# Performance work log

Measured on AMD Instinct MI355X. Metric: run time of the kernel, lower is better.

## Reference

```python
import jax, jax.numpy as jnp
import numpy as np

EPS = 1e-5  # torch BatchNorm1d default eps


def _bn(x, axes):
    # BatchNorm in training mode with gamma=1, beta=0 (torch init values):
    # normalize with biased batch statistics over the given axes.
    m = x.mean(axes, keepdims=True)
    v = x.var(axes, keepdims=True)
    return (x - m) * jax.lax.rsqrt(v + EPS)


def setup_inputs() -> dict:
    key = jax.random.key(0)
    ks = jax.random.split(key, 12)
    N, M = 50000, 12
    OF, F, E, H = 92, 64, 41, 128
    Z = 2 * F + E  # 169 = concat(node, nbr_node, edge)

    def w(k, shape, fan):
        return jax.random.normal(k, shape, jnp.float32) * np.float32(1.0 / np.sqrt(fan))

    return {
        "node_fea": jax.random.normal(ks[0], (N, OF), jnp.float32),
        "edge_fea": jax.random.uniform(ks[1], (N, M, E), dtype=jnp.float32),
        "nbr_offset": jax.random.randint(ks[2], (N, M, 3), -1, 2).astype(jnp.float32),
        "atom_pos": jax.random.uniform(ks[3], (N, 3), dtype=jnp.float32) * 10.0,
        "cells": jnp.broadcast_to(jnp.eye(3, dtype=jnp.float32) * 10.0, (N, 3, 3))
                 + jax.random.normal(ks[4], (N, 3, 3), jnp.float32) * 0.1,
        "edge_idx": jax.random.randint(ks[5], (N, M), 0, N),
        "W_emb": w(ks[6], (OF, F), OF), "b_emb": jnp.zeros((F,), jnp.float32),
        "W_pre_node": w(ks[7], (3, Z, 2 * F), Z), "b_pre_node": jnp.zeros((3, 2 * F), jnp.float32),
        "W_pre_edge": w(ks[8], (3, Z, 2 * E), Z), "b_pre_edge": jnp.zeros((3, 2 * E), jnp.float32),
        "W_dist": w(ks[9], (Z, H), Z), "b_dist": jnp.zeros((H,), jnp.float32),
        "W_const": w(ks[10], (Z, H), Z), "b_const": jnp.zeros((H,), jnp.float32),
    }


def reference(node_fea, edge_fea, nbr_offset, atom_pos, cells, edge_idx,
              W_emb, b_emb, W_pre_node, b_pre_node, W_pre_edge, b_pre_edge,
              W_dist, b_dist, W_const, b_const):
    N, M = edge_idx.shape
    lrelu = jax.nn.leaky_relu  # torch LeakyReLU default slope 0.01
    sig = jax.nn.sigmoid
    sp = jax.nn.softplus

    # get_distance: neighbor Cartesian positions via unit-cell offsets
    off_cart = jnp.einsum('nmi,nij->nmj', nbr_offset, cells)         # (N,M,3)
    diff = atom_pos[edge_idx] + off_cart - atom_pos[:, None, :]       # (N,M,3)
    distance = jnp.sqrt(jnp.sum(diff * diff, -1, keepdims=True) + 1e-12)  # (N,M,1)

    node = node_fea @ W_emb + b_emb  # embedding -> (N,64)

    for l in range(W_pre_node.shape[0]):  # n_conv = 3 ConvLayers
        nbr = node[edge_idx]  # gather (N,M,F)
        z = jnp.concatenate(
            [jnp.broadcast_to(node[:, None, :], (N, M, node.shape[-1])), nbr, edge_fea],
            axis=2)  # (N,M,169)
        # node branch: linear -> BN -> sigmoid*leakyrelu gate -> sum over M -> BN -> residual
        zn = _bn(z @ W_pre_node[l] + b_pre_node[l], (0, 1))  # (N,M,128)
        nf, nc = jnp.split(zn, 2, axis=2)
        aggr = jnp.sum(sig(nf) * lrelu(nc), axis=1)           # (N,64)
        node = lrelu(node + _bn(aggr, (0,)))
        # edge branch: linear -> BN -> gate -> BN -> residual
        ze = _bn(z @ W_pre_edge[l] + b_pre_edge[l], (0, 1))   # (N,M,82)
        ef, ec = jnp.split(ze, 2, axis=2)
        edge_fea = lrelu(edge_fea + _bn(sig(ef) * lrelu(ec), (0, 1)))

    nbr = node[edge_idx]
    bond_fea = jnp.concatenate(
        [jnp.broadcast_to(node[:, None, :], (N, M, node.shape[-1])), nbr, edge_fea],
        axis=2)  # (N,M,169)

    # n_h_dist == 1 branch: softplus(BN(linear) + distance), mean over channels
    bd = sp(_bn(bond_fea @ W_dist + b_dist, (0, 1)) + distance)
    bd = jnp.mean(bd, axis=2, keepdims=True)                  # (N,M,1)
    # n_h_const == 1 branch: softplus(BN(linear)), mean over channels, / N
    bc = sp(_bn(bond_fea @ W_const + b_const, (0, 1)))
    bc = jnp.mean(bc, axis=2, keepdims=True) / N              # (N,M,1)

    return jnp.concatenate([bd, bc], axis=2)                  # (N,M,2)
```

## Files before the change

### kernel.cpp

```cpp
#include <hip/hip_runtime.h>
#include <math.h>

#define NN 50000
#define MM 12
#define NM 600000
#define OF 92
#define FF 64
#define EE 41
#define ES 48
#define ZZ 169
#define RPB 96
#define NPB 8
#define NBLK 6250
#define KP 200
#define KSTEPS 6
#define MT 6
#define NSLICE 64
#define PSTRIDE 1024
#define TPB 512

typedef __bf16 bf16x8 __attribute__((ext_vector_type(8)));
typedef float  f32x4  __attribute__((ext_vector_type(4)));

__device__ __forceinline__ float lrelu(float x){ return fmaxf(x, 0.01f*x); }
__device__ __forceinline__ float sigm(float x){ return __builtin_amdgcn_rcpf(1.f+__expf(-x)); }
__device__ __forceinline__ float softpl(float x){ return fmaxf(x,0.f) + __logf(1.f+__expf(-fabsf(x))); }
__device__ __forceinline__ unsigned short f2bf(float f){
    __bf16 h = (__bf16)f;
    return __builtin_bit_cast(unsigned short, h);
}
__device__ __forceinline__ float b2f(unsigned short u){
    unsigned int b = ((unsigned int)u) << 16;
    return __builtin_bit_cast(float, b);
}

__global__ __launch_bounds__(256) void pack_w(const float* __restrict__ Wn,
    const float* __restrict__ We, const float* __restrict__ Wd,
    const float* __restrict__ Wc, unsigned short* __restrict__ dst)
{
    int idx = blockIdx.x*256 + threadIdx.x;
    if (idx >= 4*49152) return;
    int j    = idx & 7;
    int lane = (idx >> 3) & 63;
    int ntks = (idx >> 9) % 96;
    int L    = idx / 49152;
    int nt = ntks & 15, ks = ntks >> 4;
    int k   = ks*32 + (lane>>4)*8 + j;
    int col = nt*16 + (lane&15);
    float v = 0.f;
    if (k < ZZ) {
        if (L < 3) {
            if (col < 128)                       v = Wn[((size_t)L*ZZ + k)*128 + col];
            else if (col >= 128 && col < 128+EE) v = We[((size_t)L*ZZ + k)*82 + (col-128)];
            else if (col >= 192 && col < 192+EE) v = We[((size_t)L*ZZ + k)*82 + 41 + (col-192)];
        } else {
            if (col < 128) v = Wd[(size_t)k*128 + col];
            else           v = Wc[(size_t)k*128 + (col-128)];
        }
    }
    dst[idx] = f2bf(v);
}

__global__ __launch_bounds__(256) void k_dist(const float* __restrict__ off,
    const float* __restrict__ apos, const float* __restrict__ cells,
    const int* __restrict__ eidx, float* __restrict__ distb)
{
    int idx = blockIdx.x*256 + threadIdx.x;
    if (idx >= NM) return;
    int n = idx / MM;
    const float* o  = off + (size_t)idx*3;
    const float* cl = cells + (size_t)n*9;
    int n2 = eidx[idx];
    float o0=o[0], o1=o[1], o2=o[2];
    float dd = 1e-12f;
    #pragma unroll
    for (int j=0;j<3;j++){
        float oc = o0*cl[0*3+j] + o1*cl[1*3+j] + o2*cl[2*3+j];
        float d = apos[(size_t)n2*3+j] + oc - apos[(size_t)n*3+j];
        dd += d*d;
    }
    distb[idx] = sqrtf(dd);
}

__global__ __launch_bounds__(256) void k_cvt(const float* __restrict__ src,
    unsigned short* __restrict__ e)
{
    int idx = blockIdx.x*256 + threadIdx.x;
    if (idx >= NM*ES) return;
    int gr = idx / ES;
    int c  = idx - gr*ES;
    e[idx] = (c < EE) ? f2bf(src[(size_t)gr*EE + c]) : (unsigned short)0;
}

__global__ __launch_bounds__(256) void k_emb(const float* __restrict__ nf,
    const float* __restrict__ W, const float* __restrict__ b,
    unsigned short* __restrict__ node0)
{
    int idx = blockIdx.x*256 + threadIdx.x;
    if (idx >= NN*FF) return;
    int n = idx >> 6, c = idx & 63;
    float s = b[c];
    for (int k=0;k<OF;k++) s = fmaf(nf[(size_t)n*OF+k], W[k*FF+c], s);
    node0[idx] = f2bf(s);
}

__global__ __launch_bounds__(256) void k_red(float* __restrict__ P,
    float* __restrict__ dst, int lo, int hi)
{
    for (int c = lo + threadIdx.x; c < hi; c += 256) {
        float s = 0.f;
        #pragma unroll 8
        for (int sl = 0; sl < NSLICE; ++sl) s += P[sl*PSTRIDE + c];
        dst[c] = s;
        #pragma unroll 8
        for (int sl = 0; sl < NSLICE; ++sl) P[sl*PSTRIDE + c] = 0.f;
    }
}

__device__ __forceinline__ void stage_z(unsigned short* __restrict__ Zl,
    const unsigned short* __restrict__ node_src, const unsigned short* __restrict__ edge_src,
    const int* __restrict__ eidx, int n0, int tid)
{
    const int gr0 = n0 * MM;
    const int r0 = tid >> 3, ch = tid & 7;
    const bool two = tid < 256;
    const int r1 = r0 + 64;
    const int e0 = eidx[gr0 + r0];
    const int e1 = two ? eidx[gr0 + r1] : 0;
    const int na0 = n0 + r0 / MM;
    const int na1 = n0 + r1 / MM;
    const uint4 z4 = make_uint4(0u,0u,0u,0u);
    uint4 s0  = *(const uint4*)(node_src + (size_t)na0*FF + ch*8);
    uint4 nb0 = *(const uint4*)(node_src + (size_t)e0*FF + ch*8);
    uint4 d0 = z4, s1 = z4, nb1 = z4, d1 = z4;
    if (ch < 6) d0 = *(const uint4*)(edge_src + (size_t)(gr0+r0)*ES + ch*8);
    if (two) {
        s1  = *(const uint4*)(node_src + (size_t)na1*FF + ch*8);
        nb1 = *(const uint4*)(node_src + (size_t)e1*FF + ch*8);
        if (ch < 6) d1 = *(const uint4*)(edge_src + (size_t)(gr0+r1)*ES + ch*8);
    }
    *(uint4*)(Zl + r0*KP + ch*8)        = s0;
    *(uint4*)(Zl + r0*KP + 64 + ch*8)   = nb0;
    *(uint4*)(Zl + r0*KP + 128 + ch*8)  = d0;
    if (two) {
        *(uint4*)(Zl + r1*KP + ch*8)       = s1;
        *(uint4*)(Zl + r1*KP + 64 + ch*8)  = nb1;
        *(uint4*)(Zl + r1*KP + 128 + ch*8) = d1;
    }
}

__device__ __forceinline__ void mfma_core(const unsigned short* __restrict__ Zl,
    const unsigned short* __restrict__ Wpk, int h, int sw, int lane, f32x4 (&acc)[MT][2])
{
    const int quad = lane >> 4, li = lane & 15;
    #pragma unroll
    for (int mt=0;mt<MT;mt++){
        acc[mt][0] = (f32x4){0.f,0.f,0.f,0.f};
        acc[mt][1] = (f32x4){0.f,0.f,0.f,0.f};
    }
    const int nt0 = h*8 + sw;
    #pragma unroll 2
    for (int ks=0; ks<KSTEPS; ++ks) {
        bf16x8 bfr0 = *(const bf16x8*)(Wpk + (((ks*16 + nt0    )*64 + lane) << 3));
        bf16x8 bfr1 = *(const bf16x8*)(Wpk + (((ks*16 + nt0 + 4)*64 + lane) << 3));
        bf16x8 afr[MT];
        #pragma unroll
        for (int mt=0;mt<MT;mt++)
            afr[mt] = *(const bf16x8*)(Zl + (mt*16+li)*KP + ks*32 + quad*8);
        #pragma unroll
        for (int mt=0;mt<MT;mt++){
            acc[mt][0] = __builtin_amdgcn_mfma_f32_16x16x32_bf16(afr[mt], bfr0, acc[mt][0], 0, 0, 0);
            acc[mt][1] = __builtin_amdgcn_mfma_f32_16x16x32_bf16(afr[mt], bfr1, acc[mt][1], 0, 0, 0);
        }
    }
}

__device__ __forceinline__ void stats_epi(const f32x4 (&acc)[MT][2], int h, int sw, int lane,
    float* __restrict__ Ps)
{
    const int quad = lane>>4, li = lane&15;
    #pragma unroll
    for (int t=0;t<2;t++){
        float s=0.f, q=0.f;
        #pragma unroll
        for (int mt=0;mt<MT;mt++)
            #pragma unroll
            for (int r=0;r<4;r++){ float v = acc[mt][t][r]; s+=v; q = fmaf(v,v,q); }
        s += __shfl_xor(s,16); s += __shfl_xor(s,32);
        q += __shfl_xor(q,16); q += __shfl_xor(q,32);
        if (quad == 0) {
            int col = h*128 + t*64 + sw*16 + li;
            atomicAdd(&Ps[col], s);
            atomicAdd(&Ps[256+col], q);
        }
    }
}

__global__ __launch_bounds__(TPB,3) void k_stats(
    const unsigned short* __restrict__ node_src, const unsigned short* __restrict__ edge_src,
    const int* __restrict__ eidx, const unsigned short* __restrict__ Wpk,
    float* __restrict__ Pst)
{
    __shared__ unsigned short Zl[RPB*KP];
    const int tid = threadIdx.x, w = tid>>6, lane = tid&63;
    const int h = w>>2, sw = w&3;
    const int n0 = blockIdx.x * NPB;
    stage_z(Zl, node_src, edge_src, eidx, n0, tid);
    __syncthreads();
    f32x4 acc[MT][2];
    mfma_core(Zl, Wpk, h, sw, lane, acc);
    float* Ps = Pst + (size_t)(blockIdx.x & (NSLICE-1))*PSTRIDE;
    stats_epi(acc, h, sw, lane, Ps);
}

__global__ __launch_bounds__(TPB,3) void k_apply_re(
    const unsigned short* __restrict__ node_src, const unsigned short* __restrict__ edge_src,
    const int* __restrict__ eidx, const unsigned short* __restrict__ Wpk,
    const float* __restrict__ preS, const float* __restrict__ preQ,
    float* __restrict__ aggr, unsigned short* __restrict__ gbuf,
    float* __restrict__ Pst)
{
    __shared__ __align__(16) char smem[RPB*KP*2];
    unsigned short* Zl = (unsigned short*)smem;
    float* gL = (float*)smem;
    const int tid = threadIdx.x, w = tid>>6, lane = tid&63;
    const int quad = lane>>4, li = lane&15;
    const int h = w>>2, sw = w&3;
    const int n0 = blockIdx.x * NPB;
    const int gr0 = n0 * MM;
    stage_z(Zl, node_src, edge_src, eidx, n0, tid);
    __syncthreads();
    f32x4 acc[MT][2];
    mfma_core(Zl, Wpk, h, sw, lane, acc);
    __syncthreads();

    const int cg0 = sw*16 + li;
    float sc[2], bi[2];
    #pragma unroll
    for (int t=0;t<2;t++){
        int col = h*128 + t*64 + cg0;
        float mm = preS[col]*(1.f/(float)NM);
        float vv = preQ[col]*(1.f/(float)NM) - mm*mm;
        float is = rsqrtf(vv + 1e-5f);
        sc[t] = is; bi[t] = -mm*is;
    }
    float* Ps = Pst + (size_t)(blockIdx.x & (NSLICE-1))*PSTRIDE;

    if (h == 0) {
        #pragma unroll
        for (int mt=0;mt<MT;mt++)
            #pragma unroll
            for (int r=0;r<4;r++){
                int row = mt*16 + quad*4 + r;
                float nf = fmaf(acc[mt][0][r], sc[0], bi[0]);
                float nc = fmaf(acc[mt][1][r], sc[1], bi[1]);
                gL[row*68 + cg0] = sigm(nf) * lrelu(nc);
            }
    } else {
        const bool ce_ok = cg0 < EE;
        float pg = 0.f, pq = 0.f;
        #pragma unroll
        for (int mt=0;mt<MT;mt++)
            #pragma unroll
            for (int r=0;r<4;r++){
                int row = mt*16 + quad*4 + r;
                float ef = fmaf(acc[mt][0][r], sc[0], bi[0]);
                float ec = fmaf(acc[mt][1][r], sc[1], bi[1]);
                float gv = sigm(ef)*lrelu(ec);
                if (ce_ok) {
                    gbuf[(size_t)(gr0+row)*ES + cg0] = f2bf(gv);
                    pg += gv; pq = fmaf(gv,gv,pq);
                }
            }
        pg += __shfl_xor(pg,16); pg += __shfl_xor(pg,32);
        pq += __shfl_xor(pq,16); pq += __shfl_xor(pq,32);
        if (quad==0 && ce_ok){ atomicAdd(&Ps[640+cg0], pg); atomicAdd(&Ps[704+cg0], pq); }
    }
    __syncthreads();
    {
        float vsum = 0.f;
        #pragma unroll
        for (int jj=0;jj<MM;jj++) vsum += gL[(w*MM+jj)*68 + lane];
        aggr[(size_t)(n0+w)*64 + lane] = vsum;
        atomicAdd(&Ps[512+lane], vsum);
        atomicAdd(&Ps[576+lane], vsum*vsum);
    }
}

__global__ __launch_bounds__(256) void k_upd_node(const unsigned short* __restrict__ cur,
    const float* __restrict__ aggr, const float* __restrict__ aS,
    const float* __restrict__ aQ, unsigned short* __restrict__ nxt)
{
    int idx = blockIdx.x*256 + threadIdx.x;
    if (idx >= NN*8) return;
    int n = idx >> 3, ch = idx & 7;
    int base = n*64 + ch*8;
    float4 a0 = *(const float4*)(aggr + base);
    float4 a1 = *(const float4*)(aggr + base + 4);
    uint4 cu = *(const uint4*)(cur + base);
    unsigned short cs[8]; *(uint4*)cs = cu;
    float av[8] = {a0.x,a0.y,a0.z,a0.w,a1.x,a1.y,a1.z,a1.w};
    unsigned short os[8];
    #pragma unroll
    for (int j=0;j<8;j++){
        int c = ch*8+j;
        float mm = aS[c]*(1.f/(float)NN);
        float vv = aQ[c]*(1.f/(float)NN) - mm*mm;
        float is = rsqrtf(vv + 1e-5f);
        float v = (av[j] - mm) * is;
        os[j] = f2bf(lrelu(b2f(cs[j]) + v));
    }
    *(uint4*)(nxt + base) = *(uint4*)os;
}

__global__ __launch_bounds__(256) void k_upd_edge(unsigned short* __restrict__ e,
    const unsigned short* __restrict__ g, const float* __restrict__ gS,
    const float* __restrict__ gQ)
{
    int idx = blockIdx.x*256 + threadIdx.x;
    if (idx >= NM*6) return;
    int gr = idx / 6, ch = idx - gr*6;
    size_t base = (size_t)gr*ES + ch*8;
    uint4 eu = *(const uint4*)(e + base);
    uint4 gu = *(const uint4*)(g + base);
    unsigned short es8[8], gs8[8], os[8];
    *(uint4*)es8 = eu; *(uint4*)gs8 = gu;
    #pragma unroll
    for (int j=0;j<8;j++){
        int c = ch*8+j;
        if (c < EE) {
            float mm = gS[c]*(1.f/(float)NM);
            float vv = gQ[c]*(1.f/(float)NM) - mm*mm;
            float is = rsqrtf(vv + 1e-5f);
            float v = (b2f(gs8[j]) - mm) * is;
            os[j] = f2bf(lrelu(b2f(es8[j]) + v));
        } else {
            os[j] = es8[j];
        }
    }
    *(uint4*)(e + base) = *(uint4*)os;
}

__global__ __launch_bounds__(TPB,3) void k_final_re(
    const unsigned short* __restrict__ node_src, const unsigned short* __restrict__ edge_src,
    const int* __restrict__ eidx, const unsigned short* __restrict__ Wpk,
    const float* __restrict__ fS, const float* __restrict__ fQ,
    const float* __restrict__ distb, float* __restrict__ out)
{
    __shared__ __align__(16) char smem[RPB*KP*2];
    unsigned short* Zl = (unsigned short*)smem;
    float* bufD = (float*)smem;
    float* bufC = (float*)(smem + 8192);
    const int tid = threadIdx.x, w = tid>>6, lane = tid&63;
    const int quad = lane>>4, li = lane&15;
    const int h = w>>2, sw = w&3;
    const int n0 = blockIdx.x * NPB;
    const int gr0 = n0 * MM;
    stage_z(Zl, node_src, edge_src, eidx, n0, tid);
    __syncthreads();
    f32x4 acc[MT][2];
    mfma_core(Zl, Wpk, h, sw, lane, acc);
    __syncthreads();

    const int cg0 = sw*16 + li;
    float sc[2], bi[2];
    #pragma unroll
    for (int t=0;t<2;t++){
        int col = h*128 + t*64 + cg0;
        float mm = fS[col]*(1.f/(float)NM);
        float vv = fQ[col]*(1.f/(float)NM) - mm*mm;
        float is = rsqrtf(vv + 1e-5f);
        sc[t] = is; bi[t] = -mm*is;
    }
    const int liq = li >> 2;
    const bool wr = (li & 3) == 0;
    float* buf = (h == 0) ? bufD : bufC;
    #pragma unroll
    for (int mt=0;mt<MT;mt++)
        #pragma unroll
        for (int r=0;r<4;r++){
            int row = mt*16 + quad*4 + r;
            float v0 = fmaf(acc[mt][0][r], sc[0], bi[0]);
            float v1 = fmaf(acc[mt][1][r], sc[1], bi[1]);
            float p;
            if (h == 0) {
                float dv = distb[gr0 + row];
                p = softpl(v0 + dv) + softpl(v1 + dv);
            } else {
                p = softpl(v0) + softpl(v1);
            }
            p += __shfl_xor(p,1); p += __shfl_xor(p,2);
            if (wr) buf[row*17 + sw*4 + liq] = p;
        }
    __syncthreads();
    if (tid < 2*RPB) {
        int hh = tid >= RPB;
        int row = tid - (hh ? RPB : 0);
        const float* bsrc = hh ? bufC : bufD;
        float s = 0.f;
        #pragma unroll
        for (int t=0;t<16;t++) s += bsrc[row*17+t];
        size_t gr = gr0 + row;
        out[gr*2 + hh] = hh ? s * (1.f/128.f) * (1.f/(float)NN) : s * (1.f/128.f);
    }
}

extern "C" void kernel_launch(void* const* d_in, const int* in_sizes, int n_in,
                              void* d_out, int out_size, void* d_ws, size_t ws_size,
                              hipStream_t stream)
{
    const float* node_fea = (const float*)d_in[0];
    const float* edge_in  = (const float*)d_in[1];
    const float* nbr_off  = (const float*)d_in[2];
    const float* apos     = (const float*)d_in[3];
    const float* cells    = (const float*)d_in[4];
    const int*   eidx     = (const int*)  d_in[5];
    const float* W_emb    = (const float*)d_in[6];
    const float* b_emb    = (const float*)d_in[7];
    const float* W_pn     = (const float*)d_in[8];
    const float* W_pe     = (const float*)d_in[10];
    const float* W_dist   = (const float*)d_in[12];
    const float* W_cst    = (const float*)d_in[14];
    float* out = (float*)d_out;
    char* ws = (char*)d_ws;

    size_t o = 0;
    auto alloc = [&](size_t bytes) { char* p = ws + o; o += (bytes + 255) & ~(size_t)255; return p; };
    unsigned short* node0 = (unsigned short*)alloc((size_t)NN*FF*2);
    unsigned short* node1 = (unsigned short*)alloc((size_t)NN*FF*2);
    unsigned short* ebuf  = (unsigned short*)alloc((size_t)NM*ES*2);
    unsigned short* gbuf  = (unsigned short*)alloc((size_t)NM*ES*2);
    float* aggr  = (float*)alloc((size_t)NN*FF*4);
    float* distb = (float*)alloc((size_t)NM*4);
    unsigned short* Wpk = (unsigned short*)alloc((size_t)4*49152*2);
    float* stats = (float*)alloc(4096*4);
    float* Pst   = (float*)alloc((size_t)NSLICE*PSTRIDE*4);

    hipMemsetAsync(stats, 0, 4096*sizeof(float), stream);
    hipMemsetAsync(Pst, 0, (size_t)NSLICE*PSTRIDE*sizeof(float), stream);
    pack_w<<<(4*49152+255)/256, 256, 0, stream>>>(W_pn, W_pe, W_dist, W_cst, Wpk);
    k_dist <<<(NM+255)/256,     256, 0, stream>>>(nbr_off, apos, cells, eidx, distb);
    k_cvt  <<<(NM*ES+255)/256,  256, 0, stream>>>(edge_in, ebuf);
    k_emb  <<<(NN*FF+255)/256,  256, 0, stream>>>(node_fea, W_emb, b_emb, node0);

    const unsigned short* ncur = node0;

    for (int l=0;l<3;l++){
        float* st = stats + l*768;
        float* preS = st;       float* preQ = st+256;
        float* aSs  = st+512;   float* aQq  = st+576;
        float* gSs  = st+640;   float* gQq  = st+704;
        const unsigned short* Wl = Wpk + (size_t)l*49152;
        unsigned short* ndst = (l & 1) ? node0 : node1;

        k_stats  <<<NBLK,TPB,0,stream>>>(ncur, ebuf, eidx, Wl, Pst);
        k_red    <<<1,256,0,stream>>>(Pst, st, 0, 512);
        k_apply_re<<<NBLK,TPB,0,stream>>>(ncur, ebuf, eidx, Wl, preS, preQ,
                                          aggr, gbuf, Pst);
        k_red    <<<1,256,0,stream>>>(Pst, st, 512, 768);
        k_upd_node<<<(NN*8+255)/256,256,0,stream>>>(ncur, aggr, aSs, aQq, ndst);
        k_upd_edge<<<(NM*6+255)/256,256,0,stream>>>(ebuf, gbuf, gSs, gQq);
        ncur = ndst;
    }

    float* fSt = stats + 3*768;
    float* fS = fSt; float* fQ = fSt + 256;
    const unsigned short* Wf = Wpk + (size_t)3*49152;
    k_stats  <<<NBLK,TPB,0,stream>>>(ncur, ebuf, eidx, Wf, Pst);
    k_red    <<<1,256,0,stream>>>(Pst, fSt, 0, 512);
    k_final_re<<<NBLK,TPB,0,stream>>>(ncur, ebuf, eidx, Wf, fS, fQ, distb, out);
}
```

Baseline: 1.239 ms.

## Fuse edge BN update into stats staging and process two tiles per block

The separate edge-update kernel is removed. The edge residual BN update now runs inside the next layer's stats kernel while it stages the Z tile, and the updated edge features are written back to the edge buffer there. Each block now handles two 96-row tiles, prefetching the second tile's global loads into registers while the MFMAs for the first run, and atomics are accumulated across both tiles before being issued. This saves a full pass over the edge buffer and halves the block count. In exchange it raises register pressure from the eight uint4 prefetch registers and adds extra barriers.

```diff
diff --git a/kernel.cpp b/kernel.cpp
--- a/kernel.cpp
+++ b/kernel.cpp
@@ -11,7 +11,8 @@
 #define ZZ 169
 #define RPB 96
 #define NPB 8
-#define NBLK 6250
+#define NTILE 6250
+#define NBLK2 3125
 #define KP 200
 #define KSTEPS 6
 #define MT 6
@@ -117,46 +118,91 @@
     }
 }
 
-__device__ __forceinline__ void stage_z(unsigned short* __restrict__ Zl,
-    const unsigned short* __restrict__ node_src, const unsigned short* __restrict__ edge_src,
-    const int* __restrict__ eidx, int n0, int tid)
+__device__ __forceinline__ void stage_load(uint4* __restrict__ R,
+    const unsigned short* __restrict__ node_src, const unsigned short* __restrict__ ebuf,
+    const unsigned short* __restrict__ gbuf, const int* __restrict__ eidx,
+    int n0, int tid, bool upd)
 {
     const int gr0 = n0 * MM;
     const int r0 = tid >> 3, ch = tid & 7;
     const bool two = tid < 256;
-    const int r1 = r0 + 64;
-    const int e0 = eidx[gr0 + r0];
-    const int e1 = two ? eidx[gr0 + r1] : 0;
-    const int na0 = n0 + r0 / MM;
-    const int na1 = n0 + r1 / MM;
     const uint4 z4 = make_uint4(0u,0u,0u,0u);
-    uint4 s0  = *(const uint4*)(node_src + (size_t)na0*FF + ch*8);
-    uint4 nb0 = *(const uint4*)(node_src + (size_t)e0*FF + ch*8);
-    uint4 d0 = z4, s1 = z4, nb1 = z4, d1 = z4;
-    if (ch < 6) d0 = *(const uint4*)(edge_src + (size_t)(gr0+r0)*ES + ch*8);
+    int e0 = eidx[gr0 + r0];
+    R[0] = *(const uint4*)(node_src + (size_t)(n0 + r0/MM)*FF + ch*8);
+    R[1] = *(const uint4*)(node_src + (size_t)e0*FF + ch*8);
+    R[2] = z4; R[3] = z4; R[4] = z4; R[5] = z4; R[6] = z4; R[7] = z4;
+    if (ch < 6) {
+        R[2] = *(const uint4*)(ebuf + (size_t)(gr0+r0)*ES + ch*8);
+        if (upd) R[3] = *(const uint4*)(gbuf + (size_t)(gr0+r0)*ES + ch*8);
+    }
     if (two) {
-        s1  = *(const uint4*)(node_src + (size_t)na1*FF + ch*8);
-        nb1 = *(const uint4*)(node_src + (size_t)e1*FF + ch*8);
-        if (ch < 6) d1 = *(const uint4*)(edge_src + (size_t)(gr0+r1)*ES + ch*8);
-    }
-    *(uint4*)(Zl + r0*KP + ch*8)        = s0;
-    *(uint4*)(Zl + r0*KP + 64 + ch*8)   = nb0;
-    *(uint4*)(Zl + r0*KP + 128 + ch*8)  = d0;
+        int r1 = r0 + 64;
+        int e1 = eidx[gr0 + r1];
+        R[4] = *(const uint4*)(node_src + (size_t)(n0 + r1/MM)*FF + ch*8);
+        R[5] = *(const uint4*)(node_src + (size_t)e1*FF + ch*8);
+        if (ch < 6) {
+            R[6] = *(const uint4*)(ebuf + (size_t)(gr0+r1)*ES + ch*8);
+            if (upd) R[7] = *(const uint4*)(gbuf + (size_t)(gr0+r1)*ES + ch*8);
+        }
+    }
+}
+
+__device__ __forceinline__ uint4 upd_edge8(uint4 e, uint4 g,
+    const float* __restrict__ mmv, const float* __restrict__ isv, int ch)
+{
+    unsigned short es[8], gs[8], os[8];
+    *(uint4*)es = e; *(uint4*)gs = g;
+    #pragma unroll
+    for (int j=0;j<8;j++){
+        int c = ch*8+j;
+        if (c < EE){
+            float v = (b2f(gs[j]) - mmv[j]) * isv[j];
+            os[j] = f2bf(lrelu(b2f(es[j]) + v));
+        } else os[j] = es[j];
+    }
+    return *(uint4*)os;
+}
+
+__device__ __forceinline__ void stage_write(uint4* __restrict__ R,
+    unsigned short* __restrict__ Zl, unsigned short* __restrict__ ebuf_wb,
+    int n0, int tid, bool upd,
+    const float* __restrict__ mmv, const float* __restrict__ isv)
+{
+    const int gr0 = n0 * MM;
+    const int r0 = tid >> 3, ch = tid & 7;
+    const bool two = tid < 256;
+    uint4 d0 = R[2];
+    if (upd && ch < 6) {
+        d0 = upd_edge8(R[2], R[3], mmv, isv, ch);
+        *(uint4*)(ebuf_wb + (size_t)(gr0+r0)*ES + ch*8) = d0;
+    }
+    *(uint4*)(Zl + r0*KP + ch*8)       = R[0];
+    *(uint4*)(Zl + r0*KP + 64 + ch*8)  = R[1];
+    *(uint4*)(Zl + r0*KP + 128 + ch*8) = d0;
     if (two) {
-        *(uint4*)(Zl + r1*KP + ch*8)       = s1;
-        *(uint4*)(Zl + r1*KP + 64 + ch*8)  = nb1;
+        int r1 = r0 + 64;
+        uint4 d1 = R[6];
+        if (upd && ch < 6) {
+            d1 = upd_edge8(R[6], R[7], mmv, isv, ch);
+            *(uint4*)(ebuf_wb + (size_t)(gr0+r1)*ES + ch*8) = d1;
+        }
+        *(uint4*)(Zl + r1*KP + ch*8)       = R[4];
+        *(uint4*)(Zl + r1*KP + 64 + ch*8)  = R[5];
         *(uint4*)(Zl + r1*KP + 128 + ch*8) = d1;
     }
 }
 
+template<bool ZERO>
 __device__ __forceinline__ void mfma_core(const unsigned short* __restrict__ Zl,
     const unsigned short* __restrict__ Wpk, int h, int sw, int lane, f32x4 (&acc)[MT][2])
 {
     const int quad = lane >> 4, li = lane & 15;
-    #pragma unroll
-    for (int mt=0;mt<MT;mt++){
-        acc[mt][0] = (f32x4){0.f,0.f,0.f,0.f};
-        acc[mt][1] = (f32x4){0.f,0.f,0.f,0.f};
+    if (ZERO) {
+        #pragma unroll
+        for (int mt=0;mt<MT;mt++){
+            acc[mt][0] = (f32x4){0.f,0.f,0.f,0.f};
+            acc[mt][1] = (f32x4){0.f,0.f,0.f,0.f};
+        }
     }
     const int nt0 = h*8 + sw;
     #pragma unroll 2
@@ -197,24 +243,49 @@
 }
 
 __global__ __launch_bounds__(TPB,3) void k_stats(
-    const unsigned short* __restrict__ node_src, const unsigned short* __restrict__ edge_src,
-    const int* __restrict__ eidx, const unsigned short* __restrict__ Wpk,
+    const unsigned short* __restrict__ node_src, unsigned short* __restrict__ ebuf,
+    const unsigned short* __restrict__ gbuf, const int* __restrict__ eidx,
+    const unsigned short* __restrict__ Wpk,
+    const float* __restrict__ gS, const float* __restrict__ gQ,
     float* __restrict__ Pst)
 {
     __shared__ unsigned short Zl[RPB*KP];
     const int tid = threadIdx.x, w = tid>>6, lane = tid&63;
     const int h = w>>2, sw = w&3;
-    const int n0 = blockIdx.x * NPB;
-    stage_z(Zl, node_src, edge_src, eidx, n0, tid);
+    const bool upd = (gS != nullptr);
+    const int ch = tid & 7;
+    float mmv[8], isv[8];
+    if (upd) {
+        #pragma unroll
+        for (int j=0;j<8;j++){
+            int c = ch*8+j;
+            float mm = 0.f, is = 0.f;
+            if (c < EE) {
+                mm = gS[c]*(1.f/(float)NM);
+                float vv = gQ[c]*(1.f/(float)NM) - mm*mm;
+                is = rsqrtf(vv + 1e-5f);
+            }
+            mmv[j] = mm; isv[j] = is;
+        }
+    }
+    const int t0 = blockIdx.x * 2;
+    uint4 R[8];
+    stage_load(R, node_src, ebuf, gbuf, eidx, t0*NPB, tid, upd);
+    stage_write(R, Zl, ebuf, t0*NPB, tid, upd, mmv, isv);
     __syncthreads();
+    stage_load(R, node_src, ebuf, gbuf, eidx, (t0+1)*NPB, tid, upd);
     f32x4 acc[MT][2];
-    mfma_core(Zl, Wpk, h, sw, lane, acc);
+    mfma_core<true>(Zl, Wpk, h, sw, lane, acc);
+    __syncthreads();
+    stage_write(R, Zl, ebuf, (t0+1)*NPB, tid, upd, mmv, isv);
+    __syncthreads();
+    mfma_core<false>(Zl, Wpk, h, sw, lane, acc);
     float* Ps = Pst + (size_t)(blockIdx.x & (NSLICE-1))*PSTRIDE;
     stats_epi(acc, h, sw, lane, Ps);
 }
 
 __global__ __launch_bounds__(TPB,3) void k_apply_re(
-    const unsigned short* __restrict__ node_src, const unsigned short* __restrict__ edge_src,
+    const unsigned short* __restrict__ node_src, const unsigned short* __restrict__ ebuf,
     const int* __restrict__ eidx, const unsigned short* __restrict__ Wpk,
     const float* __restrict__ preS, const float* __restrict__ preQ,
     float* __restrict__ aggr, unsigned short* __restrict__ gbuf,
@@ -226,13 +297,13 @@
     const int tid = threadIdx.x, w = tid>>6, lane = tid&63;
     const int quad = lane>>4, li = lane&15;
     const int h = w>>2, sw = w&3;
-    const int n0 = blockIdx.x * NPB;
-    const int gr0 = n0 * MM;
-    stage_z(Zl, node_src, edge_src, eidx, n0, tid);
+    const int t0 = blockIdx.x * 2;
+
+    uint4 R[8];
+    stage_load(R, node_src, ebuf, nullptr, eidx, t0*NPB, tid, false);
+    stage_write(R, Zl, nullptr, t0*NPB, tid, false, nullptr, nullptr);
     __syncthreads();
-    f32x4 acc[MT][2];
-    mfma_core(Zl, Wpk, h, sw, lane, acc);
-    __syncthreads();
+    stage_load(R, node_src, ebuf, nullptr, eidx, (t0+1)*NPB, tid, false);
 
     const int cg0 = sw*16 + li;
     float sc[2], bi[2];
@@ -244,47 +315,62 @@
         float is = rsqrtf(vv + 1e-5f);
         sc[t] = is; bi[t] = -mm*is;
     }
+    const bool ce_ok = cg0 < EE;
     float* Ps = Pst + (size_t)(blockIdx.x & (NSLICE-1))*PSTRIDE;
-
-    if (h == 0) {
-        #pragma unroll
-        for (int mt=0;mt<MT;mt++)
+    float pg = 0.f, pq = 0.f;
+    float sAcc = 0.f, sQq = 0.f;
+
+    f32x4 acc[MT][2];
+    #pragma unroll
+    for (int tile=0; tile<2; ++tile){
+        const int n0 = (t0+tile)*NPB;
+        const int gr0 = n0 * MM;
+        mfma_core<true>(Zl, Wpk, h, sw, lane, acc);
+        __syncthreads();
+        if (h == 0) {
             #pragma unroll
-            for (int r=0;r<4;r++){
-                int row = mt*16 + quad*4 + r;
-                float nf = fmaf(acc[mt][0][r], sc[0], bi[0]);
-                float nc = fmaf(acc[mt][1][r], sc[1], bi[1]);
-                gL[row*68 + cg0] = sigm(nf) * lrelu(nc);
-            }
-    } else {
-        const bool ce_ok = cg0 < EE;
-        float pg = 0.f, pq = 0.f;
-        #pragma unroll
-        for (int mt=0;mt<MT;mt++)
+            for (int mt=0;mt<MT;mt++)
+                #pragma unroll
+                for (int r=0;r<4;r++){
+                    int row = mt*16 + quad*4 + r;
+                    float nf = fmaf(acc[mt][0][r], sc[0], bi[0]);
+                    float nc = fmaf(acc[mt][1][r], sc[1], bi[1]);
+                    gL[row*68 + cg0] = sigm(nf) * lrelu(nc);
+                }
+        } else {
             #pragma unroll
-            for (int r=0;r<4;r++){
-                int row = mt*16 + quad*4 + r;
-                float ef = fmaf(acc[mt][0][r], sc[0], bi[0]);
-                float ec = fmaf(acc[mt][1][r], sc[1], bi[1]);
-                float gv = sigm(ef)*lrelu(ec);
-                if (ce_ok) {
-                    gbuf[(size_t)(gr0+row)*ES + cg0] = f2bf(gv);
-                    pg += gv; pq = fmaf(gv,gv,pq);
+            for (int mt=0;mt<MT;mt++)
+                #pragma unroll
+                for (int r=0;r<4;r++){
+                    int row = mt*16 + quad*4 + r;
+                    float ef = fmaf(acc[mt][0][r], sc[0], bi[0]);
+                    float ec = fmaf(acc[mt][1][r], sc[1], bi[1]);
+                    float gv = sigm(ef)*lrelu(ec);
+                    if (ce_ok) {
+                        gbuf[(size_t)(gr0+row)*ES + cg0] = f2bf(gv);
+                        pg += gv; pq = fmaf(gv,gv,pq);
+                    }
                 }
-            }
-        pg += __shfl_xor(pg,16); pg += __shfl_xor(pg,32);
-        pq += __shfl_xor(pq,16); pq += __shfl_xor(pq,32);
-        if (quad==0 && ce_ok){ atomicAdd(&Ps[640+cg0], pg); atomicAdd(&Ps[704+cg0], pq); }
-    }
-    __syncthreads();
-    {
-        float vsum = 0.f;
-        #pragma unroll
-        for (int jj=0;jj<MM;jj++) vsum += gL[(w*MM+jj)*68 + lane];
-        aggr[(size_t)(n0+w)*64 + lane] = vsum;
-        atomicAdd(&Ps[512+lane], vsum);
-        atomicAdd(&Ps[576+lane], vsum*vsum);
-    }
+        }
+        __syncthreads();
+        {
+            float vsum = 0.f;
+            #pragma unroll
+            for (int jj=0;jj<MM;jj++) vsum += gL[(w*MM+jj)*68 + lane];
+            aggr[(size_t)(n0+w)*64 + lane] = vsum;
+            sAcc += vsum; sQq = fmaf(vsum,vsum,sQq);
+        }
+        if (tile == 0) {
+            __syncthreads();
+            stage_write(R, Zl, nullptr, (t0+1)*NPB, tid, false, nullptr, nullptr);
+            __syncthreads();
+        }
+    }
+    pg += __shfl_xor(pg,16); pg += __shfl_xor(pg,32);
+    pq += __shfl_xor(pq,16); pq += __shfl_xor(pq,32);
+    if (h==1 && quad==0 && ce_ok){ atomicAdd(&Ps[640+cg0], pg); atomicAdd(&Ps[704+cg0], pq); }
+    atomicAdd(&Ps[512+lane], sAcc);
+    atomicAdd(&Ps[576+lane], sQq);
 }
 
 __global__ __launch_bounds__(256) void k_upd_node(const unsigned short* __restrict__ cur,
@@ -313,36 +399,8 @@
     *(uint4*)(nxt + base) = *(uint4*)os;
 }
 
-__global__ __launch_bounds__(256) void k_upd_edge(unsigned short* __restrict__ e,
-    const unsigned short* __restrict__ g, const float* __restrict__ gS,
-    const float* __restrict__ gQ)
-{
-    int idx = blockIdx.x*256 + threadIdx.x;
-    if (idx >= NM*6) return;
-    int gr = idx / 6, ch = idx - gr*6;
-    size_t base = (size_t)gr*ES + ch*8;
-    uint4 eu = *(const uint4*)(e + base);
-    uint4 gu = *(const uint4*)(g + base);
-    unsigned short es8[8], gs8[8], os[8];
-    *(uint4*)es8 = eu; *(uint4*)gs8 = gu;
-    #pragma unroll
-    for (int j=0;j<8;j++){
-        int c = ch*8+j;
-        if (c < EE) {
-            float mm = gS[c]*(1.f/(float)NM);
-            float vv = gQ[c]*(1.f/(float)NM) - mm*mm;
-            float is = rsqrtf(vv + 1e-5f);
-            float v = (b2f(gs8[j]) - mm) * is;
-            os[j] = f2bf(lrelu(b2f(es8[j]) + v));
-        } else {
-            os[j] = es8[j];
-        }
-    }
-    *(uint4*)(e + base) = *(uint4*)os;
-}
-
 __global__ __launch_bounds__(TPB,3) void k_final_re(
-    const unsigned short* __restrict__ node_src, const unsigned short* __restrict__ edge_src,
+    const unsigned short* __restrict__ node_src, const unsigned short* __restrict__ ebuf,
     const int* __restrict__ eidx, const unsigned short* __restrict__ Wpk,
     const float* __restrict__ fS, const float* __restrict__ fQ,
     const float* __restrict__ distb, float* __restrict__ out)
@@ -354,13 +412,13 @@
     const int tid = threadIdx.x, w = tid>>6, lane = tid&63;
     const int quad = lane>>4, li = lane&15;
     const int h = w>>2, sw = w&3;
-    const int n0 = blockIdx.x * NPB;
-    const int gr0 = n0 * MM;
-    stage_z(Zl, node_src, edge_src, eidx, n0, tid);
+    const int t0 = blockIdx.x * 2;
+
+    uint4 R[8];
+    stage_load(R, node_src, ebuf, nullptr, eidx, t0*NPB, tid, false);
+    stage_write(R, Zl, nullptr, t0*NPB, tid, false, nullptr, nullptr);
     __syncthreads();
-    f32x4 acc[MT][2];
-    mfma_core(Zl, Wpk, h, sw, lane, acc);
-    __syncthreads();
+    stage_load(R, node_src, ebuf, nullptr, eidx, (t0+1)*NPB, tid, false);
 
     const int cg0 = sw*16 + li;
     float sc[2], bi[2];
@@ -374,34 +432,48 @@
     }
     const int liq = li >> 2;
     const bool wr = (li & 3) == 0;
-    float* buf = (h == 0) ? bufD : bufC;
-    #pragma unroll
-    for (int mt=0;mt<MT;mt++)
+
+    f32x4 acc[MT][2];
+    #pragma unroll
+    for (int tile=0; tile<2; ++tile){
+        const int n0 = (t0+tile)*NPB;
+        const int gr0 = n0 * MM;
+        mfma_core<true>(Zl, Wpk, h, sw, lane, acc);
+        __syncthreads();
+        float* buf = (h == 0) ? bufD : bufC;
         #pragma unroll
-        for (int r=0;r<4;r++){
-            int row = mt*16 + quad*4 + r;
-            float v0 = fmaf(acc[mt][0][r], sc[0], bi[0]);
-            float v1 = fmaf(acc[mt][1][r], sc[1], bi[1]);
-            float p;
-            if (h == 0) {
-                float dv = distb[gr0 + row];
-                p = softpl(v0 + dv) + softpl(v1 + dv);
-            } else {
-                p = softpl(v0) + softpl(v1);
+        for (int mt=0;mt<MT;mt++)
+            #pragma unroll
+            for (int r=0;r<4;r++){
+                int row = mt*16 + quad*4 + r;
+                float v0 = fmaf(acc[mt][0][r], sc[0], bi[0]);
+                float v1 = fmaf(acc[mt][1][r], sc[1], bi[1]);
+                float p;
+                if (h == 0) {
+                    float dv = distb[gr0 + row];
+                    p = softpl(v0 + dv) + softpl(v1 + dv);
+                } else {
+                    p = softpl(v0) + softpl(v1);
+                }
+                p += __shfl_xor(p,1); p += __shfl_xor(p,2);
+                if (wr) buf[row*17 + sw*4 + liq] = p;
             }
-            p += __shfl_xor(p,1); p += __shfl_xor(p,2);
-            if (wr) buf[row*17 + sw*4 + liq] = p;
-        }
-    __syncthreads();
-    if (tid < 2*RPB) {
-        int hh = tid >= RPB;
-        int row = tid - (hh ? RPB : 0);
-        const float* bsrc = hh ? bufC : bufD;
-        float s = 0.f;
-        #pragma unroll
-        for (int t=0;t<16;t++) s += bsrc[row*17+t];
-        size_t gr = gr0 + row;
-        out[gr*2 + hh] = hh ? s * (1.f/128.f) * (1.f/(float)NN) : s * (1.f/128.f);
+        __syncthreads();
+        if (tid < 2*RPB) {
+            int hh = tid >= RPB;
+            int row = tid - (hh ? RPB : 0);
+            const float* bsrc = hh ? bufC : bufD;
+            float s = 0.f;
+            #pragma unroll
+            for (int t=0;t<16;t++) s += bsrc[row*17+t];
+            size_t gr = gr0 + row;
+            out[gr*2 + hh] = hh ? s * (1.f/128.f) * (1.f/(float)NN) : s * (1.f/128.f);
+        }
+        if (tile == 0) {
+            __syncthreads();
+            stage_write(R, Zl, nullptr, (t0+1)*NPB, tid, false, nullptr, nullptr);
+            __syncthreads();
+        }
     }
 }
 
@@ -449,24 +521,26 @@
         float* st = stats + l*768;
         float* preS = st;       float* preQ = st+256;
         float* aSs  = st+512;   float* aQq  = st+576;
-        float* gSs  = st+640;   float* gQq  = st+704;
         const unsigned short* Wl = Wpk + (size_t)l*49152;
         unsigned short* ndst = (l & 1) ? node0 : node1;
-
-        k_stats  <<<NBLK,TPB,0,stream>>>(ncur, ebuf, eidx, Wl, Pst);
+        const float* gSp = (l == 0) ? nullptr : (stats + (l-1)*768 + 640);
+        const float* gQp = (l == 0) ? nullptr : (stats + (l-1)*768 + 704);
+
+        k_stats  <<<NBLK2,TPB,0,stream>>>(ncur, ebuf, gbuf, eidx, Wl, gSp, gQp, Pst);
         k_red    <<<1,256,0,stream>>>(Pst, st, 0, 512);
-        k_apply_re<<<NBLK,TPB,0,stream>>>(ncur, ebuf, eidx, Wl, preS, preQ,
-                                          aggr, gbuf, Pst);
+        k_apply_re<<<NBLK2,TPB,0,stream>>>(ncur, ebuf, eidx, Wl, preS, preQ,
+                                           aggr, gbuf, Pst);
         k_red    <<<1,256,0,stream>>>(Pst, st, 512, 768);
         k_upd_node<<<(NN*8+255)/256,256,0,stream>>>(ncur, aggr, aSs, aQq, ndst);
-        k_upd_edge<<<(NM*6+255)/256,256,0,stream>>>(ebuf, gbuf, gSs, gQq);
         ncur = ndst;
     }
 
     float* fSt = stats + 3*768;
     float* fS = fSt; float* fQ = fSt + 256;
     const unsigned short* Wf = Wpk + (size_t)3*49152;
-    k_stats  <<<NBLK,TPB,0,stream>>>(ncur, ebuf, eidx, Wf, Pst);
+    const float* gSp = stats + 2*768 + 640;
+    const float* gQp = stats + 2*768 + 704;
+    k_stats  <<<NBLK2,TPB,0,stream>>>(ncur, ebuf, gbuf, eidx, Wf, gSp, gQp, Pst);
     k_red    <<<1,256,0,stream>>>(Pst, fSt, 0, 512);
-    k_final_re<<<NBLK,TPB,0,stream>>>(ncur, ebuf, eidx, Wf, fS, fQ, distb, out);
-}
+    k_final_re<<<NBLK2,TPB,0,stream>>>(ncur, ebuf, eidx, Wf, fS, fQ, distb, out);
+}
```

Result: slower. 1.380 ms (+11.5%).

## Fuse edge update into stats staging and shrink shared Z tile layout

Applied to the files above, without the earlier changes.

Removes the separate edge-update kernel by applying the BN-gated residual edge update inside the next layer's stats kernel during staging, writing the updated edge buffer back in place. The shared-memory Z tile is split into per-node self features (8 rows, shared by the 12 neighbours via a divide-by-12 row map), neighbour features and edge features. This cuts the LDS footprint and the redundant self-feature loads. It also vectorises the edge conversion kernel to 8-wide stores and fully unrolls the K loop. In exchange, the stats kernel does extra global traffic and ALU work, and register pressure rises from the unroll and the per-thread normalisation constants.

```diff
diff --git a/kernel.cpp b/kernel.cpp
--- a/kernel.cpp
+++ b/kernel.cpp
@@ -11,13 +11,16 @@
 #define ZZ 169
 #define RPB 96
 #define NPB 8
-#define NBLK 6250
-#define KP 200
+#define NTILE 6250
 #define KSTEPS 6
 #define MT 6
 #define NSLICE 64
 #define PSTRIDE 1024
 #define TPB 512
+#define Z1OFF 0
+#define Z2OFF 13824
+#define Z0OFF 27648
+#define SMEMB 28800
 
 typedef __bf16 bf16x8 __attribute__((ext_vector_type(8)));
 typedef float  f32x4  __attribute__((ext_vector_type(4)));
@@ -86,10 +89,17 @@
     unsigned short* __restrict__ e)
 {
     int idx = blockIdx.x*256 + threadIdx.x;
-    if (idx >= NM*ES) return;
-    int gr = idx / ES;
-    int c  = idx - gr*ES;
-    e[idx] = (c < EE) ? f2bf(src[(size_t)gr*EE + c]) : (unsigned short)0;
+    if (idx >= NM*6) return;
+    int gr = idx / 6;
+    int ch = idx - gr*6;
+    const float* s = src + (size_t)gr*EE + ch*8;
+    unsigned short os[8];
+    #pragma unroll
+    for (int j=0;j<8;j++){
+        int c = ch*8+j;
+        os[j] = (c < EE) ? f2bf(s[j]) : (unsigned short)0;
+    }
+    *(uint4*)(e + (size_t)gr*ES + ch*8) = *(uint4*)os;
 }
 
 __global__ __launch_bounds__(256) void k_emb(const float* __restrict__ nf,
@@ -117,56 +127,105 @@
     }
 }
 
-__device__ __forceinline__ void stage_z(unsigned short* __restrict__ Zl,
-    const unsigned short* __restrict__ node_src, const unsigned short* __restrict__ edge_src,
-    const int* __restrict__ eidx, int n0, int tid)
-{
+__device__ __forceinline__ uint4 upd_edge8(uint4 e, uint4 g,
+    const float* __restrict__ mmv, const float* __restrict__ isv, int ch)
+{
+    unsigned short es[8], gs[8], os[8];
+    *(uint4*)es = e; *(uint4*)gs = g;
+    #pragma unroll
+    for (int j=0;j<8;j++){
+        int c = ch*8+j;
+        if (c < EE){
+            float v = (b2f(gs[j]) - mmv[j]) * isv[j];
+            os[j] = f2bf(lrelu(b2f(es[j]) + v));
+        } else os[j] = es[j];
+    }
+    return *(uint4*)os;
+}
+
+template<bool UPD>
+__device__ __forceinline__ void stage_z(char* smem,
+    const unsigned short* __restrict__ node_src, unsigned short* __restrict__ ebuf,
+    const unsigned short* __restrict__ gbuf, const int* __restrict__ eidx,
+    int n0, int tid, const float* __restrict__ mmv, const float* __restrict__ isv)
+{
+    unsigned short* Z1 = (unsigned short*)(smem + Z1OFF);
+    unsigned short* Z2 = (unsigned short*)(smem + Z2OFF);
+    unsigned short* Z0 = (unsigned short*)(smem + Z0OFF);
     const int gr0 = n0 * MM;
     const int r0 = tid >> 3, ch = tid & 7;
     const bool two = tid < 256;
     const int r1 = r0 + 64;
-    const int e0 = eidx[gr0 + r0];
-    const int e1 = two ? eidx[gr0 + r1] : 0;
-    const int na0 = n0 + r0 / MM;
-    const int na1 = n0 + r1 / MM;
-    const uint4 z4 = make_uint4(0u,0u,0u,0u);
-    uint4 s0  = *(const uint4*)(node_src + (size_t)na0*FF + ch*8);
+    int e0 = eidx[gr0 + r0];
     uint4 nb0 = *(const uint4*)(node_src + (size_t)e0*FF + ch*8);
-    uint4 d0 = z4, s1 = z4, nb1 = z4, d1 = z4;
-    if (ch < 6) d0 = *(const uint4*)(edge_src + (size_t)(gr0+r0)*ES + ch*8);
+    *(uint4*)(Z1 + r0*72 + ch*8) = nb0;
     if (two) {
-        s1  = *(const uint4*)(node_src + (size_t)na1*FF + ch*8);
-        nb1 = *(const uint4*)(node_src + (size_t)e1*FF + ch*8);
-        if (ch < 6) d1 = *(const uint4*)(edge_src + (size_t)(gr0+r1)*ES + ch*8);
-    }
-    *(uint4*)(Zl + r0*KP + ch*8)        = s0;
-    *(uint4*)(Zl + r0*KP + 64 + ch*8)   = nb0;
-    *(uint4*)(Zl + r0*KP + 128 + ch*8)  = d0;
-    if (two) {
-        *(uint4*)(Zl + r1*KP + ch*8)       = s1;
-        *(uint4*)(Zl + r1*KP + 64 + ch*8)  = nb1;
-        *(uint4*)(Zl + r1*KP + 128 + ch*8) = d1;
-    }
-}
-
-__device__ __forceinline__ void mfma_core(const unsigned short* __restrict__ Zl,
+        int e1 = eidx[gr0 + r1];
+        uint4 nb1 = *(const uint4*)(node_src + (size_t)e1*FF + ch*8);
+        *(uint4*)(Z1 + r1*72 + ch*8) = nb1;
+    }
+    {
+        uint4 v = make_uint4(0u,0u,0u,0u);
+        if (ch < 6) {
+            v = *(const uint4*)(ebuf + (size_t)(gr0+r0)*ES + ch*8);
+            if (UPD) {
+                uint4 g = *(const uint4*)(gbuf + (size_t)(gr0+r0)*ES + ch*8);
+                v = upd_edge8(v, g, mmv, isv, ch);
+                *(uint4*)(ebuf + (size_t)(gr0+r0)*ES + ch*8) = v;
+            }
+        }
+        *(uint4*)(Z2 + r0*72 + ch*8) = v;
+        if (two) {
+            uint4 v1 = make_uint4(0u,0u,0u,0u);
+            if (ch < 6) {
+                v1 = *(const uint4*)(ebuf + (size_t)(gr0+r1)*ES + ch*8);
+                if (UPD) {
+                    uint4 g1 = *(const uint4*)(gbuf + (size_t)(gr0+r1)*ES + ch*8);
+                    v1 = upd_edge8(v1, g1, mmv, isv, ch);
+                    *(uint4*)(ebuf + (size_t)(gr0+r1)*ES + ch*8) = v1;
+                }
+            }
+            *(uint4*)(Z2 + r1*72 + ch*8) = v1;
+        }
+    }
+    if (tid >= 448) {
+        int nd = (tid - 448) >> 3;
+        uint4 s = *(const uint4*)(node_src + (size_t)(n0+nd)*FF + ch*8);
+        *(uint4*)(Z0 + nd*72 + ch*8) = s;
+    }
+}
+
+__device__ __forceinline__ void mfma_core(const char* smem,
     const unsigned short* __restrict__ Wpk, int h, int sw, int lane, f32x4 (&acc)[MT][2])
 {
     const int quad = lane >> 4, li = lane & 15;
+    const unsigned short* Z1 = (const unsigned short*)(smem + Z1OFF);
+    const unsigned short* Z2 = (const unsigned short*)(smem + Z2OFF);
+    const unsigned short* Z0 = (const unsigned short*)(smem + Z0OFF);
     #pragma unroll
     for (int mt=0;mt<MT;mt++){
         acc[mt][0] = (f32x4){0.f,0.f,0.f,0.f};
         acc[mt][1] = (f32x4){0.f,0.f,0.f,0.f};
     }
+    int rd12[MT];
+    #pragma unroll
+    for (int mt=0;mt<MT;mt++) rd12[mt] = ((mt*16 + li) * 2731) >> 15;
     const int nt0 = h*8 + sw;
-    #pragma unroll 2
+    #pragma unroll
     for (int ks=0; ks<KSTEPS; ++ks) {
         bf16x8 bfr0 = *(const bf16x8*)(Wpk + (((ks*16 + nt0    )*64 + lane) << 3));
         bf16x8 bfr1 = *(const bf16x8*)(Wpk + (((ks*16 + nt0 + 4)*64 + lane) << 3));
         bf16x8 afr[MT];
         #pragma unroll
-        for (int mt=0;mt<MT;mt++)
-            afr[mt] = *(const bf16x8*)(Zl + (mt*16+li)*KP + ks*32 + quad*8);
+        for (int mt=0;mt<MT;mt++){
+            int row = mt*16 + li;
+            if (ks < 2)
+                afr[mt] = *(const bf16x8*)(Z0 + rd12[mt]*72 + ks*32 + quad*8);
+            else if (ks < 4)
+                afr[mt] = *(const bf16x8*)(Z1 + row*72 + (ks-2)*32 + quad*8);
+            else
+                afr[mt] = *(const bf16x8*)(Z2 + row*72 + (ks-4)*32 + quad*8);
+        }
         #pragma unroll
         for (int mt=0;mt<MT;mt++){
             acc[mt][0] = __builtin_amdgcn_mfma_f32_16x16x32_bf16(afr[mt], bfr0, acc[mt][0], 0, 0, 0);
@@ -196,42 +255,77 @@
     }
 }
 
-__global__ __launch_bounds__(TPB,3) void k_stats(
-    const unsigned short* __restrict__ node_src, const unsigned short* __restrict__ edge_src,
+template<bool UPD>
+__device__ __forceinline__ void k_stats_body(
+    const unsigned short* __restrict__ node_src, unsigned short* __restrict__ ebuf,
+    const unsigned short* __restrict__ gbuf, const int* __restrict__ eidx,
+    const unsigned short* __restrict__ Wpk,
+    const float* __restrict__ gS, const float* __restrict__ gQ,
+    float* __restrict__ Pst)
+{
+    __shared__ __align__(16) char smem[SMEMB];
+    const int tid = threadIdx.x, w = tid>>6, lane = tid&63;
+    const int h = w>>2, sw = w&3;
+    const int ch = tid & 7;
+    float mmv[8], isv[8];
+    if (UPD) {
+        #pragma unroll
+        for (int j=0;j<8;j++){
+            int c = ch*8+j;
+            float mm = 0.f, is = 0.f;
+            if (c < EE) {
+                mm = gS[c]*(1.f/(float)NM);
+                float vv = gQ[c]*(1.f/(float)NM) - mm*mm;
+                is = rsqrtf(vv + 1e-5f);
+            }
+            mmv[j] = mm; isv[j] = is;
+        }
+    }
+    const int n0 = blockIdx.x * NPB;
+    stage_z<UPD>(smem, node_src, ebuf, gbuf, eidx, n0, tid, mmv, isv);
+    __syncthreads();
+    f32x4 acc[MT][2];
+    mfma_core(smem, Wpk, h, sw, lane, acc);
+    float* Ps = Pst + (size_t)(blockIdx.x & (NSLICE-1))*PSTRIDE;
+    stats_epi(acc, h, sw, lane, Ps);
+}
+
+__global__ __launch_bounds__(TPB,3) void k_stats0(
+    const unsigned short* __restrict__ node_src, unsigned short* __restrict__ ebuf,
     const int* __restrict__ eidx, const unsigned short* __restrict__ Wpk,
     float* __restrict__ Pst)
 {
-    __shared__ unsigned short Zl[RPB*KP];
-    const int tid = threadIdx.x, w = tid>>6, lane = tid&63;
-    const int h = w>>2, sw = w&3;
-    const int n0 = blockIdx.x * NPB;
-    stage_z(Zl, node_src, edge_src, eidx, n0, tid);
-    __syncthreads();
-    f32x4 acc[MT][2];
-    mfma_core(Zl, Wpk, h, sw, lane, acc);
-    float* Ps = Pst + (size_t)(blockIdx.x & (NSLICE-1))*PSTRIDE;
-    stats_epi(acc, h, sw, lane, Ps);
+    k_stats_body<false>(node_src, ebuf, nullptr, eidx, Wpk, nullptr, nullptr, Pst);
+}
+
+__global__ __launch_bounds__(TPB,3) void k_stats_u(
+    const unsigned short* __restrict__ node_src, unsigned short* __restrict__ ebuf,
+    const unsigned short* __restrict__ gbuf, const int* __restrict__ eidx,
+    const unsigned short* __restrict__ Wpk,
+    const float* __restrict__ gS, const float* __restrict__ gQ,
+    float* __restrict__ Pst)
+{
+    k_stats_body<true>(node_src, ebuf, gbuf, eidx, Wpk, gS, gQ, Pst);
 }
 
 __global__ __launch_bounds__(TPB,3) void k_apply_re(
-    const unsigned short* __restrict__ node_src, const unsigned short* __restrict__ edge_src,
+    const unsigned short* __restrict__ node_src, unsigned short* __restrict__ ebuf,
     const int* __restrict__ eidx, const unsigned short* __restrict__ Wpk,
     const float* __restrict__ preS, const float* __restrict__ preQ,
     float* __restrict__ aggr, unsigned short* __restrict__ gbuf,
     float* __restrict__ Pst)
 {
-    __shared__ __align__(16) char smem[RPB*KP*2];
-    unsigned short* Zl = (unsigned short*)smem;
+    __shared__ __align__(16) char smem[SMEMB];
     float* gL = (float*)smem;
     const int tid = threadIdx.x, w = tid>>6, lane = tid&63;
     const int quad = lane>>4, li = lane&15;
     const int h = w>>2, sw = w&3;
     const int n0 = blockIdx.x * NPB;
     const int gr0 = n0 * MM;
-    stage_z(Zl, node_src, edge_src, eidx, n0, tid);
+    stage_z<false>(smem, node_src, ebuf, nullptr, eidx, n0, tid, nullptr, nullptr);
     __syncthreads();
     f32x4 acc[MT][2];
-    mfma_core(Zl, Wpk, h, sw, lane, acc);
+    mfma_core(smem, Wpk, h, sw, lane, acc);
     __syncthreads();
 
     const int cg0 = sw*16 + li;
@@ -244,6 +338,7 @@
         float is = rsqrtf(vv + 1e-5f);
         sc[t] = is; bi[t] = -mm*is;
     }
+    const bool ce_ok = cg0 < EE;
     float* Ps = Pst + (size_t)(blockIdx.x & (NSLICE-1))*PSTRIDE;
 
     if (h == 0) {
@@ -257,7 +352,6 @@
                 gL[row*68 + cg0] = sigm(nf) * lrelu(nc);
             }
     } else {
-        const bool ce_ok = cg0 < EE;
         float pg = 0.f, pq = 0.f;
         #pragma unroll
         for (int mt=0;mt<MT;mt++)
@@ -313,42 +407,13 @@
     *(uint4*)(nxt + base) = *(uint4*)os;
 }
 
-__global__ __launch_bounds__(256) void k_upd_edge(unsigned short* __restrict__ e,
-    const unsigned short* __restrict__ g, const float* __restrict__ gS,
-    const float* __restrict__ gQ)
-{
-    int idx = blockIdx.x*256 + threadIdx.x;
-    if (idx >= NM*6) return;
-    int gr = idx / 6, ch = idx - gr*6;
-    size_t base = (size_t)gr*ES + ch*8;
-    uint4 eu = *(const uint4*)(e + base);
-    uint4 gu = *(const uint4*)(g + base);
-    unsigned short es8[8], gs8[8], os[8];
-    *(uint4*)es8 = eu; *(uint4*)gs8 = gu;
-    #pragma unroll
-    for (int j=0;j<8;j++){
-        int c = ch*8+j;
-        if (c < EE) {
-            float mm = gS[c]*(1.f/(float)NM);
-            float vv = gQ[c]*(1.f/(float)NM) - mm*mm;
-            float is = rsqrtf(vv + 1e-5f);
-            float v = (b2f(gs8[j]) - mm) * is;
-            os[j] = f2bf(lrelu(b2f(es8[j]) + v));
-        } else {
-            os[j] = es8[j];
-        }
-    }
-    *(uint4*)(e + base) = *(uint4*)os;
-}
-
 __global__ __launch_bounds__(TPB,3) void k_final_re(
-    const unsigned short* __restrict__ node_src, const unsigned short* __restrict__ edge_src,
+    const unsigned short* __restrict__ node_src, unsigned short* __restrict__ ebuf,
     const int* __restrict__ eidx, const unsigned short* __restrict__ Wpk,
     const float* __restrict__ fS, const float* __restrict__ fQ,
     const float* __restrict__ distb, float* __restrict__ out)
 {
-    __shared__ __align__(16) char smem[RPB*KP*2];
-    unsigned short* Zl = (unsigned short*)smem;
+    __shared__ __align__(16) char smem[SMEMB];
     float* bufD = (float*)smem;
     float* bufC = (float*)(smem + 8192);
     const int tid = threadIdx.x, w = tid>>6, lane = tid&63;
@@ -356,10 +421,10 @@
     const int h = w>>2, sw = w&3;
     const int n0 = blockIdx.x * NPB;
     const int gr0 = n0 * MM;
-    stage_z(Zl, node_src, edge_src, eidx, n0, tid);
+    stage_z<false>(smem, node_src, ebuf, nullptr, eidx, n0, tid, nullptr, nullptr);
     __syncthreads();
     f32x4 acc[MT][2];
-    mfma_core(Zl, Wpk, h, sw, lane, acc);
+    mfma_core(smem, Wpk, h, sw, lane, acc);
     __syncthreads();
 
     const int cg0 = sw*16 + li;
@@ -440,7 +505,7 @@
     hipMemsetAsync(Pst, 0, (size_t)NSLICE*PSTRIDE*sizeof(float), stream);
     pack_w<<<(4*49152+255)/256, 256, 0, stream>>>(W_pn, W_pe, W_dist, W_cst, Wpk);
     k_dist <<<(NM+255)/256,     256, 0, stream>>>(nbr_off, apos, cells, eidx, distb);
-    k_cvt  <<<(NM*ES+255)/256,  256, 0, stream>>>(edge_in, ebuf);
+    k_cvt  <<<(NM*6+255)/256,   256, 0, stream>>>(edge_in, ebuf);
     k_emb  <<<(NN*FF+255)/256,  256, 0, stream>>>(node_fea, W_emb, b_emb, node0);
 
     const unsigned short* ncur = node0;
@@ -449,24 +514,33 @@
         float* st = stats + l*768;
         float* preS = st;       float* preQ = st+256;
         float* aSs  = st+512;   float* aQq  = st+576;
-        float* gSs  = st+640;   float* gQq  = st+704;
         const unsigned short* Wl = Wpk + (size_t)l*49152;
         unsigned short* ndst = (l & 1) ? node0 : node1;
 
-        k_stats  <<<NBLK,TPB,0,stream>>>(ncur, ebuf, eidx, Wl, Pst);
+        if (l == 0) {
+            k_stats0 <<<NTILE,TPB,0,stream>>>((const unsigned short*)ncur, ebuf, eidx, Wl, Pst);
+        } else {
+            const float* gSp = stats + (l-1)*768 + 640;
+            const float* gQp = stats + (l-1)*768 + 704;
+            k_stats_u<<<NTILE,TPB,0,stream>>>((const unsigned short*)ncur, ebuf, gbuf, eidx,
+                                              Wl, gSp, gQp, Pst);
+        }
         k_red    <<<1,256,0,stream>>>(Pst, st, 0, 512);
-        k_apply_re<<<NBLK,TPB,0,stream>>>(ncur, ebuf, eidx, Wl, preS, preQ,
-                                          aggr, gbuf, Pst);
+        k_apply_re<<<NTILE,TPB,0,stream>>>((const unsigned short*)ncur, ebuf, eidx, Wl,
+                                           preS, preQ, aggr, gbuf, Pst);
         k_red    <<<1,256,0,stream>>>(Pst, st, 512, 768);
         k_upd_node<<<(NN*8+255)/256,256,0,stream>>>(ncur, aggr, aSs, aQq, ndst);
-        k_upd_edge<<<(NM*6+255)/256,256,0,stream>>>(ebuf, gbuf, gSs, gQq);
         ncur = ndst;
     }
 
     float* fSt = stats + 3*768;
     float* fS = fSt; float* fQ = fSt + 256;
     const unsigned short* Wf = Wpk + (size_t)3*49152;
-    k_stats  <<<NBLK,TPB,0,stream>>>(ncur, ebuf, eidx, Wf, Pst);
+    const float* gSp = stats + 2*768 + 640;
+    const float* gQp = stats + 2*768 + 704;
+    k_stats_u<<<NTILE,TPB,0,stream>>>((const unsigned short*)ncur, ebuf, gbuf, eidx,
+                                      Wf, gSp, gQp, Pst);
     k_red    <<<1,256,0,stream>>>(Pst, fSt, 0, 512);
-    k_final_re<<<NBLK,TPB,0,stream>>>(ncur, ebuf, eidx, Wf, fS, fQ, distb, out);
-}
+    k_final_re<<<NTILE,TPB,0,stream>>>((const unsigned short*)ncur, ebuf, eidx, Wf,
+                                       fS, fQ, distb, out);
+}
```

Result: faster. 1.191 ms (-3.8%).
